# Kernel optimization log

Hardware: AMD Instinct MI355X
Metric: run time of the kernel (lower is better)

Reference implementation:

```python
import jax, jax.numpy as jnp
import numpy as np

B, N, C = 4, 2048, 1024


def setup_inputs() -> dict:
    key = jax.random.key(0)
    ks = jax.random.split(key, 5)
    s = 1.0 / np.sqrt(C)
    return {
        "event_f": jax.random.normal(ks[0], (B, N, C), dtype=jnp.float32),
        "img_f": jax.random.normal(ks[1], (B, N, C), dtype=jnp.float32),
        "Wq": jax.random.normal(ks[2], (C, C), dtype=jnp.float32) * s,
        "bq": jnp.zeros((C,), dtype=jnp.float32),
        "Wk": jax.random.normal(ks[3], (C, C), dtype=jnp.float32) * s,
        "bk": jnp.zeros((C,), dtype=jnp.float32),
        "Wv": jax.random.normal(ks[4], (C, C), dtype=jnp.float32) * s,
        "bv": jnp.zeros((C,), dtype=jnp.float32),
    }


def reference(event_f, img_f, Wq, bq, Wk, bk, Wv, bv):
    # pointwise projections (conv_query/key/val as 1x1 / Linear C->C)
    q = jnp.einsum("bnc,cd->bnd", event_f, Wq) + bq  # [B,N,C]
    k = jnp.einsum("bnc,cd->bnd", img_f, Wk) + bk
    v = jnp.einsum("bnc,cd->bnd", img_f, Wv) + bv
    scale = 1.0 / jnp.sqrt(jnp.asarray(q.shape[-1], dtype=q.dtype))
    scores = jnp.einsum("bqc,bkc->bqk", q, k) * scale  # [B,N,N]
    p_attn = jax.nn.softmax(scores, axis=-1)
    return jnp.einsum("bqk,bkc->bqc", p_attn, v)  # [B,N,C]
```

## Files before the change

kernel.cpp:

```cpp
#include <hip/hip_runtime.h>
#include <hip/hip_bf16.h>
#include <stdint.h>

typedef __bf16 bf16;
typedef __attribute__((ext_vector_type(8))) __bf16 bf16x8;
typedef __attribute__((ext_vector_type(4))) float f32x4;

typedef __attribute__((address_space(3))) char* lds_ptr;
typedef const __attribute__((address_space(1))) char* glb_ptr;

#define BZ 4
#define NN 2048
#define CC 1024

__device__ __forceinline__ void gload_lds16(const bf16* g, bf16* l) {
    __builtin_amdgcn_global_load_lds((glb_ptr)g, (lds_ptr)l, 16, 0, 0);
}

__device__ __forceinline__ void bar() {
    asm volatile("" ::: "memory");
    __builtin_amdgcn_s_barrier();
    asm volatile("" ::: "memory");
}

__global__ void cvt_f32_bf16(const float* __restrict__ in, bf16* __restrict__ out, int n8) {
    int i = blockIdx.x * blockDim.x + threadIdx.x;
    if (i >= n8) return;
    const float4* p = (const float4*)in;
    float4 a = p[2 * i], b = p[2 * i + 1];
    bf16x8 o;
    o[0] = (bf16)a.x; o[1] = (bf16)a.y; o[2] = (bf16)a.z; o[3] = (bf16)a.w;
    o[4] = (bf16)b.x; o[5] = (bf16)b.y; o[6] = (bf16)b.z; o[7] = (bf16)b.w;
    *(bf16x8*)(out + 8 * (size_t)i) = o;
}

__global__ void transposeW(const float* __restrict__ W, bf16* __restrict__ Wt) {
    __shared__ bf16 t[32][33];
    int d0 = blockIdx.x * 32, c0 = blockIdx.y * 32;
    int tx = threadIdx.x, ty = threadIdx.y;
#pragma unroll
    for (int i = 0; i < 4; i++)
        t[ty + 8 * i][tx] = (bf16)W[(size_t)(c0 + ty + 8 * i) * CC + d0 + tx];
    __syncthreads();
#pragma unroll
    for (int i = 0; i < 4; i++)
        Wt[(size_t)(d0 + ty + 8 * i) * CC + c0 + tx] = t[tx][ty + 8 * i];
}

__global__ void transposeV(const bf16* __restrict__ KVb, bf16* __restrict__ VT) {
    __shared__ bf16 t[32][33];
    int b = blockIdx.z;
    int n0 = blockIdx.x * 32, c0 = blockIdx.y * 32;
    const bf16* Vb = KVb + (size_t)b * NN * (2 * CC) + CC;
    bf16* Tb = VT + (size_t)b * CC * NN;
    int tx = threadIdx.x, ty = threadIdx.y;
#pragma unroll
    for (int i = 0; i < 4; i++)
        t[ty + 8 * i][tx] = Vb[(size_t)(n0 + ty + 8 * i) * (2 * CC) + c0 + tx];
    __syncthreads();
#pragma unroll
    for (int i = 0; i < 4; i++)
        Tb[(size_t)(c0 + ty + 8 * i) * NN + n0 + tx] = t[tx][ty + 8 * i];
}

__global__ void concat_bias(const float* __restrict__ a, const float* __restrict__ b,
                            float* __restrict__ o) {
    int i = blockIdx.x * blockDim.x + threadIdx.x;
    o[i] = (i < CC) ? a[i] : b[i - CC];
}


#define STAGE_A(kt_, hh_)                                                        \
    do {                                                                         \
        int _kt = (kt_);                                                         \
        if (_kt < nkt) {                                                         \
            const bf16* _s = gAs + (size_t)((hh_)*128) * lda + (size_t)_kt * 64; \
            bf16* _d = &LA[_kt & 1][((hh_)*128 + wid * 16) * 64];                \
            gload_lds16(_s, _d);                                                 \
            gload_lds16(_s + (size_t)8 * lda, _d + 8 * 64);                      \
        }                                                                        \
    } while (0)

#define STAGE_B(kt_, hh_)                                                          \
    do {                                                                           \
        int _kt = (kt_);                                                           \
        if (_kt < nkt) {                                                           \
            const bf16* _s = gBs + (size_t)((hh_) * (BN / 2)) * ldb +              \
                             (size_t)_kt * 64;                                     \
            bf16* _d = &LB[_kt & 1][((hh_) * (BN / 2) + wid * (BN / 16)) * 64];    \
            gload_lds16(_s, _d);                                                   \
            if (NJ == 2) gload_lds16(_s + (size_t)8 * ldb, _d + 8 * 64);           \
        }                                                                          \
    } while (0)

#define LDA_FRAG(buf_, mh_)                                                      \
    do {                                                                         \
        _Pragma("unroll") for (int _i = 0; _i < 4; ++_i)                         \
            _Pragma("unroll") for (int _ks = 0; _ks < 2; ++_ks)                  \
                a[_i][_ks] = *(const bf16x8*)&LA[buf_][                          \
                    (wm + (mh_)*64 + _i * 16 + fr) * 64 +                        \
                    (((_ks * 4 + hi) ^ lo) * 8)];                                \
    } while (0)

#define LDB_FRAG(buf_, nh_, dst_)                                                \
    do {                                                                         \
        _Pragma("unroll") for (int _j = 0; _j < NJ; ++_j)                        \
            _Pragma("unroll") for (int _ks = 0; _ks < 2; ++_ks)                  \
                dst_[_j][_ks] = *(const bf16x8*)&LB[buf_][                       \
                    (wn + (nh_) * (NJ * 16) + _j * 16 + fr) * 64 +               \
                    (((_ks * 4 + hi) ^ lo) * 8)];                                \
    } while (0)

#define MMQ(mh_, nh_, b_)                                                        \
    do {                                                                         \
        __builtin_amdgcn_s_setprio(1);                                           \
        _Pragma("unroll") for (int _i = 0; _i < 4; ++_i)                         \
            _Pragma("unroll") for (int _j = 0; _j < NJ; ++_j)                    \
                _Pragma("unroll") for (int _ks = 0; _ks < 2; ++_ks)              \
                    acc[(mh_)*4 + _i][(nh_)*NJ + _j] =                           \
                        __builtin_amdgcn_mfma_f32_16x16x32_bf16(                 \
                            a[_i][_ks], b_[_j][_ks],                             \
                            acc[(mh_)*4 + _i][(nh_)*NJ + _j], 0, 0, 0);          \
        __builtin_amdgcn_s_setprio(0);                                           \
    } while (0)

#define VM_STEADY()                                                              \
    do {                                                                         \
        if (NJ == 2)                                                             \
            asm volatile("s_waitcnt vmcnt(6)" ::: "memory");                     \
        else                                                                     \
            asm volatile("s_waitcnt vmcnt(4)" ::: "memory");                     \
    } while (0)

template <int BN, bool OUT_F32>
__global__ __launch_bounds__(512, 2) void gemm8(
    const bf16* __restrict__ A, int lda,
    const bf16* __restrict__ Bt, int ldb,
    void* __restrict__ Cout, int ldc,
    const float* __restrict__ bias, float scale,
    long long sA, long long sB, long long sC, int nkt) {
    constexpr int NJ = BN / 128;
    __shared__ __align__(16) bf16 LA[2][256 * 64];
    __shared__ __align__(16) bf16 LB[2][BN * 64];

    const int nx = gridDim.x, ny = gridDim.y;
    const int nwg = nx * ny * gridDim.z;
    const int orig = blockIdx.x + nx * (blockIdx.y + ny * blockIdx.z);
    const int q = nwg >> 3, r = nwg & 7;
    const int xcd = orig & 7, land = orig >> 3;
    const int swz = (xcd < r ? xcd * (q + 1) : r * (q + 1) + (xcd - r) * q) + land;
    const int bx = swz % nx;
    const int tmp = swz / nx;
    const int by = tmp % ny, bz = tmp / ny;

    A += (size_t)bz * sA;
    Bt += (size_t)bz * sB;
    const int m0 = by * 256, n0 = bx * BN;
    const int t = threadIdx.x, wid = t >> 6, lane = t & 63;
    const int wm = (wid >> 2) * 128, wn = (wid & 3) * (BN / 4);
    const int fr = lane & 15, hi = lane >> 4, lo = lane & 7;
    f32x4 acc[8][2 * NJ] = {};

    const int srow = lane >> 3;
    const int schunk = lo ^ srow;
    const bf16* gAs = A + (size_t)(m0 + wid * 16 + srow) * lda + schunk * 8;
    const bf16* gBs = Bt + (size_t)(n0 + wid * (BN / 16) + srow) * ldb + schunk * 8;

    STAGE_A(0, 0); STAGE_A(0, 1); STAGE_B(0, 0); STAGE_B(0, 1);
    STAGE_B(1, 0); STAGE_A(1, 0); STAGE_B(1, 1);
    VM_STEADY();
    bar();

    bf16x8 a[4][2], b0[NJ][2], b1[NJ][2];
    for (int kt = 0; kt < nkt; ++kt) {
        const int buf = kt & 1;
        LDA_FRAG(buf, 0);
        LDB_FRAG(buf, 0, b0);
        STAGE_A(kt + 1, 1);
        MMQ(0, 0, b0);
        bar();
        LDB_FRAG(buf, 1, b1);
        MMQ(0, 1, b1);
        bar();
        LDA_FRAG(buf, 1);
        STAGE_B(kt + 2, 0);
        MMQ(1, 1, b1);
        bar();
        STAGE_A(kt + 2, 0);
        STAGE_B(kt + 2, 1);
        MMQ(1, 0, b0);
        if (kt + 2 < nkt)
            VM_STEADY();
        else
            asm volatile("s_waitcnt vmcnt(0)" ::: "memory");
        bar();
    }

    const int rq = hi * 4;
#pragma unroll
    for (int mh = 0; mh < 2; mh++)
#pragma unroll
        for (int i = 0; i < 4; i++)
#pragma unroll
            for (int nh = 0; nh < 2; nh++)
#pragma unroll
                for (int j = 0; j < NJ; j++) {
                    int col = n0 + wn + nh * (NJ * 16) + j * 16 + fr;
                    float bb = bias ? bias[col] : 0.f;
                    f32x4 v = acc[mh * 4 + i][nh * NJ + j];
                    int row = m0 + wm + mh * 64 + i * 16 + rq;
#pragma unroll
                    for (int rr = 0; rr < 4; rr++) {
                        float o = v[rr] * scale + bb;
                        if (OUT_F32)
                            ((float*)Cout)[(size_t)bz * sC + (size_t)(row + rr) * ldc + col] = o;
                        else
                            ((bf16*)Cout)[(size_t)bz * sC + (size_t)(row + rr) * ldc + col] = (bf16)o;
                    }
                }
}

__global__ __launch_bounds__(256) void softmax_rows(bf16* __restrict__ S) {
    const size_t row = blockIdx.x;
    bf16* p = S + row * (size_t)NN;
    const int t = threadIdx.x;
    bf16x8 vv = *(const bf16x8*)(p + t * 8);
    float f[8];
    float m = -1e30f;
#pragma unroll
    for (int i = 0; i < 8; i++) { f[i] = (float)vv[i]; m = fmaxf(m, f[i]); }
#pragma unroll
    for (int off = 32; off; off >>= 1) m = fmaxf(m, __shfl_xor(m, off));
    __shared__ float redm[4], reds[4];
    int wave = t >> 6, lane = t & 63;
    if (lane == 0) redm[wave] = m;
    __syncthreads();
    m = fmaxf(fmaxf(redm[0], redm[1]), fmaxf(redm[2], redm[3]));
    float s = 0.f;
#pragma unroll
    for (int i = 0; i < 8; i++) { f[i] = __expf(f[i] - m); s += f[i]; }
#pragma unroll
    for (int off = 32; off; off >>= 1) s += __shfl_xor(s, off);
    if (lane == 0) reds[wave] = s;
    __syncthreads();
    s = reds[0] + reds[1] + reds[2] + reds[3];
    float inv = 1.f / s;
    bf16x8 ov;
#pragma unroll
    for (int i = 0; i < 8; i++) ov[i] = (bf16)(f[i] * inv);
    *(bf16x8*)(p + t * 8) = ov;
}

extern "C" void kernel_launch(void* const* d_in, const int* in_sizes, int n_in,
                              void* d_out, int out_size, void* d_ws, size_t ws_size,
                              hipStream_t stream) {
    const float* event_f = (const float*)d_in[0];
    const float* img_f   = (const float*)d_in[1];
    const float* Wq = (const float*)d_in[2];
    const float* bq = (const float*)d_in[3];
    const float* Wk = (const float*)d_in[4];
    const float* bk = (const float*)d_in[5];
    const float* Wv = (const float*)d_in[6];
    const float* bv = (const float*)d_in[7];
    float* out = (float*)d_out;

    bf16* ws = (bf16*)d_ws;
    const size_t MC = (size_t)BZ * NN * CC;
    bf16* Ebf  = ws;
    bf16* Ibf  = ws + MC;
    bf16* S    = ws;
    size_t off = 2 * MC;
    bf16* Wqt  = ws + off; off += (size_t)CC * CC;
    bf16* Wkvt = ws + off; off += (size_t)2 * CC * CC;
    bf16* Qb   = ws + off; off += MC;
    bf16* KVb  = ws + off; off += 2 * MC;
    bf16* VT   = ws + off; off += MC;
    float* bkv = (float*)(ws + off);

    {
        int n8 = (int)(MC / 8);
        cvt_f32_bf16<<<dim3((n8 + 255) / 256), dim3(256), 0, stream>>>(event_f, Ebf, n8);
        cvt_f32_bf16<<<dim3((n8 + 255) / 256), dim3(256), 0, stream>>>(img_f, Ibf, n8);
    }
    {
        dim3 g(CC / 32, CC / 32), b(32, 8);
        transposeW<<<g, b, 0, stream>>>(Wq, Wqt);
        transposeW<<<g, b, 0, stream>>>(Wk, Wkvt);
        transposeW<<<g, b, 0, stream>>>(Wv, Wkvt + (size_t)CC * CC);
        concat_bias<<<dim3(8), dim3(256), 0, stream>>>(bk, bv, bkv);
    }
    gemm8<128, false><<<dim3(CC / 128, (BZ * NN) / 256, 1), dim3(512), 0, stream>>>(
        Ebf, CC, Wqt, CC, Qb, CC, bq, 1.f, 0, 0, 0, CC / 64);
    gemm8<256, false><<<dim3((2 * CC) / 256, (BZ * NN) / 256, 1), dim3(512), 0, stream>>>(
        Ibf, CC, Wkvt, CC, KVb, 2 * CC, bkv, 1.f, 0, 0, 0, CC / 64);
    {
        dim3 g(NN / 32, CC / 32, BZ), b(32, 8);
        transposeV<<<g, b, 0, stream>>>(KVb, VT);
    }
    gemm8<256, false><<<dim3(NN / 256, NN / 256, BZ), dim3(512), 0, stream>>>(
        Qb, CC, KVb, 2 * CC, S, NN, nullptr, 1.f / 32.f,
        (long long)NN * CC, (long long)NN * 2 * CC, (long long)NN * NN, CC / 64);
    softmax_rows<<<dim3(BZ * NN), dim3(256), 0, stream>>>(S);
    gemm8<128, true><<<dim3(CC / 128, NN / 256, BZ), dim3(512), 0, stream>>>(
        S, NN, VT, NN, out, CC, nullptr, 1.f,
        (long long)NN * NN, (long long)CC * NN, (long long)NN * CC, NN / 64);
}
```

Before: 190.4 us.

## Compute V transposed directly via GEMM and batch Q/K projections and prep kernels

Result: faster. 181.7 us (-4.6%).

```diff
diff --git a/kernel.cpp b/kernel.cpp
--- a/kernel.cpp
+++ b/kernel.cpp
@@ -23,19 +23,29 @@
     asm volatile("" ::: "memory");
 }
 
-__global__ void cvt_f32_bf16(const float* __restrict__ in, bf16* __restrict__ out, int n8) {
+__global__ void cvt2_f32_bf16(const float* __restrict__ a, const float* __restrict__ b,
+                              bf16* __restrict__ oa, bf16* __restrict__ ob, int n8) {
     int i = blockIdx.x * blockDim.x + threadIdx.x;
-    if (i >= n8) return;
-    const float4* p = (const float4*)in;
-    float4 a = p[2 * i], b = p[2 * i + 1];
+    if (i >= 2 * n8) return;
+    const float4* p;
+    bf16* dst;
+    int j;
+    if (i < n8) { p = (const float4*)a; dst = oa; j = i; }
+    else        { p = (const float4*)b; dst = ob; j = i - n8; }
+    float4 x = p[2 * j], y = p[2 * j + 1];
     bf16x8 o;
-    o[0] = (bf16)a.x; o[1] = (bf16)a.y; o[2] = (bf16)a.z; o[3] = (bf16)a.w;
-    o[4] = (bf16)b.x; o[5] = (bf16)b.y; o[6] = (bf16)b.z; o[7] = (bf16)b.w;
-    *(bf16x8*)(out + 8 * (size_t)i) = o;
-}
-
-__global__ void transposeW(const float* __restrict__ W, bf16* __restrict__ Wt) {
+    o[0] = (bf16)x.x; o[1] = (bf16)x.y; o[2] = (bf16)x.z; o[3] = (bf16)x.w;
+    o[4] = (bf16)y.x; o[5] = (bf16)y.y; o[6] = (bf16)y.z; o[7] = (bf16)y.w;
+    *(bf16x8*)(dst + 8 * (size_t)j) = o;
+}
+
+__global__ void transposeW3(const float* __restrict__ W0, const float* __restrict__ W1,
+                            const float* __restrict__ W2, bf16* __restrict__ T0,
+                            bf16* __restrict__ T1, bf16* __restrict__ T2) {
     __shared__ bf16 t[32][33];
+    const int z = blockIdx.z;
+    const float* W = z == 0 ? W0 : (z == 1 ? W1 : W2);
+    bf16* Wt = z == 0 ? T0 : (z == 1 ? T1 : T2);
     int d0 = blockIdx.x * 32, c0 = blockIdx.y * 32;
     int tx = threadIdx.x, ty = threadIdx.y;
 #pragma unroll
@@ -45,22 +55,6 @@
 #pragma unroll
     for (int i = 0; i < 4; i++)
         Wt[(size_t)(d0 + ty + 8 * i) * CC + c0 + tx] = t[tx][ty + 8 * i];
-}
-
-__global__ void transposeV(const bf16* __restrict__ KVb, bf16* __restrict__ VT) {
-    __shared__ bf16 t[32][33];
-    int b = blockIdx.z;
-    int n0 = blockIdx.x * 32, c0 = blockIdx.y * 32;
-    const bf16* Vb = KVb + (size_t)b * NN * (2 * CC) + CC;
-    bf16* Tb = VT + (size_t)b * CC * NN;
-    int tx = threadIdx.x, ty = threadIdx.y;
-#pragma unroll
-    for (int i = 0; i < 4; i++)
-        t[ty + 8 * i][tx] = Vb[(size_t)(n0 + ty + 8 * i) * (2 * CC) + c0 + tx];
-    __syncthreads();
-#pragma unroll
-    for (int i = 0; i < 4; i++)
-        Tb[(size_t)(c0 + ty + 8 * i) * NN + n0 + tx] = t[tx][ty + 8 * i];
 }
 
 __global__ void concat_bias(const float* __restrict__ a, const float* __restrict__ b,
@@ -132,12 +126,12 @@
             asm volatile("s_waitcnt vmcnt(4)" ::: "memory");                     \
     } while (0)
 
-template <int BN, bool OUT_F32>
+template <int BN, int BIAS_MODE, bool OUT_F32>
 __global__ __launch_bounds__(512, 2) void gemm8(
     const bf16* __restrict__ A, int lda,
     const bf16* __restrict__ Bt, int ldb,
     void* __restrict__ Cout, int ldc,
-    const float* __restrict__ bias, float scale,
+    const float* __restrict__ bias, long long sBias, float scale,
     long long sA, long long sB, long long sC, int nkt) {
     constexpr int NJ = BN / 128;
     __shared__ __align__(16) bf16 LA[2][256 * 64];
@@ -206,12 +200,13 @@
 #pragma unroll
                 for (int j = 0; j < NJ; j++) {
                     int col = n0 + wn + nh * (NJ * 16) + j * 16 + fr;
-                    float bb = bias ? bias[col] : 0.f;
+                    float bb = (BIAS_MODE == 1) ? bias[bz * sBias + col] : 0.f;
                     f32x4 v = acc[mh * 4 + i][nh * NJ + j];
                     int row = m0 + wm + mh * 64 + i * 16 + rq;
 #pragma unroll
                     for (int rr = 0; rr < 4; rr++) {
                         float o = v[rr] * scale + bb;
+                        if (BIAS_MODE == 2) o += bias[row + rr];
                         if (OUT_F32)
                             ((float*)Cout)[(size_t)bz * sC + (size_t)(row + rr) * ldc + col] = o;
                         else
@@ -266,42 +261,37 @@
 
     bf16* ws = (bf16*)d_ws;
     const size_t MC = (size_t)BZ * NN * CC;
+    const size_t CCsq = (size_t)CC * CC;
     bf16* Ebf  = ws;
     bf16* Ibf  = ws + MC;
     bf16* S    = ws;
     size_t off = 2 * MC;
-    bf16* Wqt  = ws + off; off += (size_t)CC * CC;
-    bf16* Wkvt = ws + off; off += (size_t)2 * CC * CC;
+    bf16* Wqkt = ws + off; off += 2 * CCsq;
+    bf16* Wvt  = ws + off; off += CCsq;
     bf16* Qb   = ws + off; off += MC;
-    bf16* KVb  = ws + off; off += 2 * MC;
+    bf16* Kb   = ws + off; off += MC;
     bf16* VT   = ws + off; off += MC;
-    float* bkv = (float*)(ws + off);
+    float* bqk = (float*)(ws + off);
 
     {
         int n8 = (int)(MC / 8);
-        cvt_f32_bf16<<<dim3((n8 + 255) / 256), dim3(256), 0, stream>>>(event_f, Ebf, n8);
-        cvt_f32_bf16<<<dim3((n8 + 255) / 256), dim3(256), 0, stream>>>(img_f, Ibf, n8);
+        cvt2_f32_bf16<<<dim3((2 * n8 + 255) / 256), dim3(256), 0, stream>>>(
+            event_f, img_f, Ebf, Ibf, n8);
     }
-    {
-        dim3 g(CC / 32, CC / 32), b(32, 8);
-        transposeW<<<g, b, 0, stream>>>(Wq, Wqt);
-        transposeW<<<g, b, 0, stream>>>(Wk, Wkvt);
-        transposeW<<<g, b, 0, stream>>>(Wv, Wkvt + (size_t)CC * CC);
-        concat_bias<<<dim3(8), dim3(256), 0, stream>>>(bk, bv, bkv);
-    }
-    gemm8<128, false><<<dim3(CC / 128, (BZ * NN) / 256, 1), dim3(512), 0, stream>>>(
-        Ebf, CC, Wqt, CC, Qb, CC, bq, 1.f, 0, 0, 0, CC / 64);
-    gemm8<256, false><<<dim3((2 * CC) / 256, (BZ * NN) / 256, 1), dim3(512), 0, stream>>>(
-        Ibf, CC, Wkvt, CC, KVb, 2 * CC, bkv, 1.f, 0, 0, 0, CC / 64);
-    {
-        dim3 g(NN / 32, CC / 32, BZ), b(32, 8);
-        transposeV<<<g, b, 0, stream>>>(KVb, VT);
-    }
-    gemm8<256, false><<<dim3(NN / 256, NN / 256, BZ), dim3(512), 0, stream>>>(
-        Qb, CC, KVb, 2 * CC, S, NN, nullptr, 1.f / 32.f,
-        (long long)NN * CC, (long long)NN * 2 * CC, (long long)NN * NN, CC / 64);
+    transposeW3<<<dim3(CC / 32, CC / 32, 3), dim3(32, 8), 0, stream>>>(
+        Wq, Wk, Wv, Wqkt, Wqkt + CCsq, Wvt);
+    concat_bias<<<dim3(8), dim3(256), 0, stream>>>(bq, bk, bqk);
+    gemm8<128, 1, false><<<dim3(CC / 128, (BZ * NN) / 256, 2), dim3(512), 0, stream>>>(
+        Ebf, CC, Wqkt, CC, Qb, CC, bqk, CC, 1.f,
+        (long long)MC, (long long)CCsq, (long long)MC, CC / 64);
+    gemm8<128, 2, false><<<dim3(NN / 128, CC / 256, BZ), dim3(512), 0, stream>>>(
+        Wvt, CC, Ibf, CC, VT, NN, bv, 0, 1.f,
+        0, (long long)NN * CC, (long long)CC * NN, CC / 64);
+    gemm8<256, 0, false><<<dim3(NN / 256, NN / 256, BZ), dim3(512), 0, stream>>>(
+        Qb, CC, Kb, CC, S, NN, nullptr, 0, 1.f / 32.f,
+        (long long)NN * CC, (long long)NN * CC, (long long)NN * NN, CC / 64);
     softmax_rows<<<dim3(BZ * NN), dim3(256), 0, stream>>>(S);
-    gemm8<128, true><<<dim3(CC / 128, NN / 256, BZ), dim3(512), 0, stream>>>(
-        S, NN, VT, NN, out, CC, nullptr, 1.f,
+    gemm8<128, 0, true><<<dim3(CC / 128, NN / 256, BZ), dim3(512), 0, stream>>>(
+        S, NN, VT, NN, out, CC, nullptr, 0, 1.f,
         (long long)NN * NN, (long long)CC * NN, (long long)NN * CC, NN / 64);
 }
```
